# Optimization experiments

Measured on AMD Instinct MI355X. Metric: run time of the kernel, lower is better.

## Reference

```python
import jax, jax.numpy as jnp
import numpy as np

# Static conv config (matches init_kwargs)
STRIDE = (1, 1, 1)
PAD = (1, 1, 1)
DIL = (1, 1, 1)
DG = 1  # deformable groups


def setup_inputs() -> dict:
    key = jax.random.key(0)
    k1, k2, k3 = jax.random.split(key, 3)
    N, Cin, T, H, W = 2, 32, 8, 56, 56
    Cout, kT, kH, kW = 64, 3, 3, 3
    x = jax.random.normal(k1, (N, Cin, T, H, W), dtype=jnp.float32)
    # offset channels = DG * 3 * kT*kH*kW = 81 ; layout [N, dg*K*3, To, Ho, Wo]
    offset = jax.random.normal(k2, (N, DG * 3 * kT * kH * kW, T, H, W), dtype=jnp.float32)
    stdv = 1.0 / np.sqrt(Cin * kT * kH * kW)
    weight = jax.random.uniform(k3, (Cout, Cin, kT, kH, kW), dtype=jnp.float32, minval=-stdv, maxval=stdv)
    bias = jnp.zeros((Cout,), dtype=jnp.float32)
    return {"x": x, "offset": offset, "weight": weight, "bias": bias}


def _deform_conv3d(x, offset, weight, bias):
    N, C, T, H, W = x.shape
    Co, _, kT, kH, kW = weight.shape
    K = kT * kH * kW
    st, sh, sw = STRIDE
    pt_, ph_, pw_ = PAD
    dt_, dh_, dw_ = DIL
    To = (T + 2 * pt_ - (dt_ * (kT - 1) + 1)) // st + 1
    Ho = (H + 2 * ph_ - (dh_ * (kH - 1) + 1)) // sh + 1
    Wo = (W + 2 * pw_ - (dw_ * (kW - 1) + 1)) // sw + 1
    Cg = C // DG
    # offsets: [N, DG, K, 3(dt,dh,dw), To, Ho, Wo]
    off = offset.reshape(N, DG, K, 3, To, Ho, Wo)
    kt, kh, kw = [g.reshape(-1) for g in jnp.meshgrid(
        jnp.arange(kT), jnp.arange(kH), jnp.arange(kW), indexing='ij')]
    # base sampling grid per kernel tap: [K, To, Ho, Wo] via broadcasting
    bt = (jnp.arange(To) * st - pt_)[None, :, None, None] + (kt * dt_)[:, None, None, None]
    bh = (jnp.arange(Ho) * sh - ph_)[None, None, :, None] + (kh * dh_)[:, None, None, None]
    bw = (jnp.arange(Wo) * sw - pw_)[None, None, None, :] + (kw * dw_)[:, None, None, None]
    # fractional sampling positions: [N, DG, K, To, Ho, Wo]
    pt = bt[None, None] + off[:, :, :, 0]
    ph = bh[None, None] + off[:, :, :, 1]
    pw = bw[None, None] + off[:, :, :, 2]
    t0f, h0f, w0f = jnp.floor(pt), jnp.floor(ph), jnp.floor(pw)
    lt, lh, lw = pt - t0f, ph - h0f, pw - w0f
    t0 = t0f.astype(jnp.int32)
    h0 = h0f.astype(jnp.int32)
    w0 = w0f.astype(jnp.int32)
    x_flat = x.reshape(N, DG, Cg, T * H * W)
    acc = jnp.zeros((N, DG, Cg, K, To, Ho, Wo), dtype=x.dtype)
    for ct in (0, 1):
        ti = t0 + ct
        wt = lt if ct else (1.0 - lt)
        for ch in (0, 1):
            hi = h0 + ch
            wh = lh if ch else (1.0 - lh)
            for cw in (0, 1):
                wi = w0 + cw
                ww = lw if cw else (1.0 - lw)
                valid = ((ti >= 0) & (ti < T) & (hi >= 0) & (hi < H) & (wi >= 0) & (wi < W))
                idx = (jnp.clip(ti, 0, T - 1) * H + jnp.clip(hi, 0, H - 1)) * W + jnp.clip(wi, 0, W - 1)
                v = jnp.take_along_axis(x_flat, idx.reshape(N, DG, 1, -1), axis=3)
                v = v.reshape(N, DG, Cg, K, To, Ho, Wo)
                wgt = (wt * wh * ww * valid.astype(x.dtype))[:, :, None]  # [N,DG,1,K,To,Ho,Wo]
                acc = acc + v * wgt
    w_r = weight.reshape(Co, DG, Cg, K)
    out = jnp.einsum('ogck,ngcktuv->notuv', w_r, acc)
    if bias.size > 0:
        out = out + bias[None, :, None, None, None]
    return out


def reference(x, offset, weight, bias):
    return _deform_conv3d(x, offset, weight, bias)
```

## Files before the change

### kernel.cpp

```cpp
#include <hip/hip_runtime.h>
#include <hip/hip_fp16.h>

#define CIN   32
#define COUT  64
#define TT    8
#define HH    56
#define WW    56
#define KK    27
#define SP    (TT * HH * WW)
#define NB    2
#define NBLK  784
#define DBLK  1568
#define KSPLIT 14

typedef __attribute__((ext_vector_type(8))) _Float16 half8;
typedef __attribute__((ext_vector_type(4))) float    f32x4;

#define WF_OFF   0
#define XTH_OFF  (128 << 10)

__global__ __launch_bounds__(256) void prep_kernel(const float* __restrict__ x,
                                                   const float* __restrict__ w,
                                                   __half* __restrict__ xTh,
                                                   __half* __restrict__ wf) {
    const int b = blockIdx.x;
    const int t = threadIdx.x;
    if (b < NBLK) {
        __shared__ float sm[CIN][65];
        const int s0 = b * 64, n = s0 / SP, sp0 = s0 % SP;
#pragma unroll
        for (int it = 0; it < 8; ++it) {
            const int idx = it * 256 + t, c = idx >> 6, l = idx & 63;
            sm[c][l] = x[((size_t)n * CIN + c) * SP + sp0 + l];
        }
        __syncthreads();
#pragma unroll
        for (int it = 0; it < 4; ++it) {
            const int idx = it * 256 + t, l = idx >> 4, cp = idx & 15;
            ((__half2*)xTh)[((size_t)n * SP + sp0 + l) * (CIN / 2) + cp] =
                __floats2half2_rn(sm[2 * cp][l], sm[2 * cp + 1][l]);
        }
    } else {
        const int k = b - NBLK;
#pragma unroll
        for (int it = 0; it < 8; ++it) {
            const int idx  = it * 256 + t;
            const int j    = idx & 7;
            const int lane = (idx >> 3) & 63;
            const int ct   = (idx >> 9) & 3;
            const int co   = ct * 16 + (lane & 15);
            const int c    = (lane >> 4) * 8 + j;
            wf[(((size_t)k * 4 + ct) * 64 + lane) * 8 + j] =
                __float2half(w[((size_t)co * CIN + c) * KK + k]);
        }
    }
}

__global__ __launch_bounds__(256, 3) void dconv3d_kernel(const __half* __restrict__ xTh,
                                                         const float* __restrict__ off,
                                                         const __half* __restrict__ wf,
                                                         const float* __restrict__ bias,
                                                         float* __restrict__ out) {
    __shared__ __align__(16) char smem[81 * 32 * 4];
    float (*offs)[32] = reinterpret_cast<float(*)[32]>(smem);
    float (*cmb)[2][64] = reinterpret_cast<float(*)[2][64]>(smem);

    const int t    = threadIdx.x;
    const int lane = t & 63;
    const int wv   = t >> 6;
    const int wpos = wv & 1;
    const int half = wv >> 1;

    const int posI = lane >> 2;
    const int cgI  = lane & 3;
    const int jg   = lane >> 4;

    const int bp_addr = (((lane & 15) << 2) | jg) << 2;

    const int sb  = (blockIdx.x & 7) * 196 + (blockIdx.x >> 3);
    const int s0  = sb * 32;
    const int n   = s0 / SP;
    const int spb = s0 % SP;

    {
        const float* offbase = off + ((size_t)n * (3 * KK)) * SP + spb;
        for (int i = t; i < 81 * 8; i += 256) {
            const int row = i >> 3, q = i & 7;
            *(float4*)&offs[row][q * 4] = *(const float4*)(offbase + (size_t)row * SP + q * 4);
        }
    }
    __syncthreads();

    const int sp = spb + wpos * 16 + posI;
    const int to = sp / (HH * WW);
    const int hw = sp % (HH * WW);
    const int ho = hw / WW;
    const int wo = hw % WW;
    const int pl = wpos * 16 + posI;

    f32x4 acc[4];
#pragma unroll
    for (int ct = 0; ct < 4; ++ct)
#pragma unroll
        for (int r = 0; r < 4; ++r)
            acc[ct][r] = half ? 0.f : bias[ct * 16 + jg * 4 + r];

    const __half* xn = xTh + (size_t)n * SP * CIN;

    float4 g[2][8];
    float  cw[2][8];

    auto issue = [&](int k, int b) {
        const int kt  = k / 9;
        const int khh = (k / 3) % 3;
        const int kww = k % 3;

        const float pt_ = (float)(to - 1 + kt)  + offs[k * 3 + 0][pl];
        const float ph_ = (float)(ho - 1 + khh) + offs[k * 3 + 1][pl];
        const float pw_ = (float)(wo - 1 + kww) + offs[k * 3 + 2][pl];

        const float ft = floorf(pt_), fh = floorf(ph_), fw = floorf(pw_);
        const float lt = pt_ - ft, lh = ph_ - fh, lw = pw_ - fw;
        const int t0 = (int)ft, h0 = (int)fh, w0 = (int)fw;
        const int t1 = t0 + 1, h1 = h0 + 1, w1 = w0 + 1;

        float awt[2], awh[2], aww[2];
        int   it2[2], ih2[2], iw2[2];
        awt[0] = ((unsigned)t0 < TT) ? (1.f - lt) : 0.f;
        awt[1] = ((unsigned)t1 < TT) ? lt : 0.f;
        it2[0] = min(max(t0, 0), TT - 1);  it2[1] = min(max(t1, 0), TT - 1);
        awh[0] = ((unsigned)h0 < HH) ? (1.f - lh) : 0.f;
        awh[1] = ((unsigned)h1 < HH) ? lh : 0.f;
        ih2[0] = min(max(h0, 0), HH - 1);  ih2[1] = min(max(h1, 0), HH - 1);
        aww[0] = ((unsigned)w0 < WW) ? (1.f - lw) : 0.f;
        aww[1] = ((unsigned)w1 < WW) ? lw : 0.f;
        iw2[0] = min(max(w0, 0), WW - 1);  iw2[1] = min(max(w1, 0), WW - 1);

        const int dT   = (it2[1] - it2[0]) * (HH * WW);
        const int dH   = (ih2[1] - ih2[0]) * WW;
        const int dW   = iw2[1] - iw2[0];
        const int base = (it2[0] * HH + ih2[0]) * WW + iw2[0];

        int a[8];
        a[0] = base;           a[1] = base + dW;
        a[2] = base + dH;      a[3] = a[2] + dW;
        a[4] = base + dT;      a[5] = a[4] + dW;
        a[6] = a[4] + dH;      a[7] = a[6] + dW;
#pragma unroll
        for (int ci = 0; ci < 8; ++ci) {
            const int i0 = ci >> 2, i1 = (ci >> 1) & 1, i2 = ci & 1;
            cw[b][ci] = awt[i0] * awh[i1] * aww[i2];
        }
#pragma unroll
        for (int ci = 0; ci < 8; ++ci)
            g[b][ci] = *(const float4*)(xn + (size_t)a[ci] * CIN + cgI * 8);
    };

    auto consume = [&](int b, half8 af0, half8 af1, half8 af2, half8 af3) {
        __half2 vacc[4];
#pragma unroll
        for (int j = 0; j < 4; ++j) vacc[j] = __floats2half2_rn(0.f, 0.f);
#pragma unroll
        for (int ci = 0; ci < 8; ++ci) {
            const __half2* uh = (const __half2*)&g[b][ci];
            const __half2 cw2 = __float2half2_rn(cw[b][ci]);
            vacc[0] = __hfma2(cw2, uh[0], vacc[0]);
            vacc[1] = __hfma2(cw2, uh[1], vacc[1]);
            vacc[2] = __hfma2(cw2, uh[2], vacc[2]);
            vacc[3] = __hfma2(cw2, uh[3], vacc[3]);
        }
        union { __half2 h2[4]; int i[4]; half8 h8; } u, v;
#pragma unroll
        for (int d = 0; d < 4; ++d) u.h2[d] = vacc[d];
#pragma unroll
        for (int d = 0; d < 4; ++d)
            v.i[d] = __builtin_amdgcn_ds_bpermute(bp_addr, u.i[d]);
        const half8 bfrag = v.h8;
        acc[0] = __builtin_amdgcn_mfma_f32_16x16x32_f16(af0, bfrag, acc[0], 0, 0, 0);
        acc[1] = __builtin_amdgcn_mfma_f32_16x16x32_f16(af1, bfrag, acc[1], 0, 0, 0);
        acc[2] = __builtin_amdgcn_mfma_f32_16x16x32_f16(af2, bfrag, acc[2], 0, 0, 0);
        acc[3] = __builtin_amdgcn_mfma_f32_16x16x32_f16(af3, bfrag, acc[3], 0, 0, 0);
    };

    if (half == 0) {
        issue(0, 0);
#pragma unroll
        for (int k = 0; k < KSPLIT; ++k) {
            const int cur = k & 1;
            const __half* wp = wf + ((size_t)k * 256 + lane) * 8;
            const half8 af0 = *(const half8*)(wp);
            const half8 af1 = *(const half8*)(wp + 512);
            const half8 af2 = *(const half8*)(wp + 1024);
            const half8 af3 = *(const half8*)(wp + 1536);
            if (k + 1 < KSPLIT) issue(k + 1, cur ^ 1);
            consume(cur, af0, af1, af2, af3);
        }
    } else {
        issue(KSPLIT, 0);
#pragma unroll
        for (int k = KSPLIT; k < KK; ++k) {
            const int cur = (k - KSPLIT) & 1;
            const __half* wp = wf + ((size_t)k * 256 + lane) * 8;
            const half8 af0 = *(const half8*)(wp);
            const half8 af1 = *(const half8*)(wp + 512);
            const half8 af2 = *(const half8*)(wp + 1024);
            const half8 af3 = *(const half8*)(wp + 1536);
            if (k + 1 < KK) issue(k + 1, cur ^ 1);
            consume(cur, af0, af1, af2, af3);
        }
    }

    __syncthreads();
    if (half == 1) {
#pragma unroll
        for (int ct = 0; ct < 4; ++ct)
#pragma unroll
            for (int r = 0; r < 4; ++r) cmb[ct * 4 + r][wpos][lane] = acc[ct][r];
    }
    __syncthreads();
    if (half == 0) {
#pragma unroll
        for (int ct = 0; ct < 4; ++ct)
#pragma unroll
            for (int r = 0; r < 4; ++r) {
                const int co = ct * 16 + jg * 4 + r;
                out[((size_t)n * COUT + co) * SP + spb + wpos * 16 + (lane & 15)] =
                    acc[ct][r] + cmb[ct * 4 + r][wpos][lane];
            }
    }
}

extern "C" void kernel_launch(void* const* d_in, const int* in_sizes, int n_in,
                              void* d_out, int out_size, void* d_ws, size_t ws_size,
                              hipStream_t stream) {
    const float* x    = (const float*)d_in[0];
    const float* off  = (const float*)d_in[1];
    const float* w    = (const float*)d_in[2];
    const float* bias = (const float*)d_in[3];
    float* out        = (float*)d_out;

    __half* wf  = (__half*)((char*)d_ws + WF_OFF);
    __half* xTh = (__half*)((char*)d_ws + XTH_OFF);

    prep_kernel<<<NBLK + KK, 256, 0, stream>>>(x, w, xTh, wf);
    dconv3d_kernel<<<DBLK, 256, 0, stream>>>(xTh, off, wf, bias, out);
}
```

Measured before the change: 121.5 us.

## Remap lanes to MFMA B-fragment layout, drop bpermute, raise occupancy

Lanes are remapped so that each lane gathers the channel slice and position that it later feeds directly as its MFMA B fragment. This removes the four ds_bpermute cross-lane shuffles per kernel tap. The launch bounds minimum blocks per CU is raised from 3 to 4, and sched_barrier fences pin the prefetch issue between the weight loads and the consume step. The higher occupancy target may force register spills, and the fences limit how freely the compiler can interleave instructions.

Result: slower. 156.6 us (+28.9%).

```diff
diff --git a/kernel.cpp b/kernel.cpp
--- a/kernel.cpp
+++ b/kernel.cpp
@@ -56,7 +56,7 @@
     }
 }
 
-__global__ __launch_bounds__(256, 3) void dconv3d_kernel(const __half* __restrict__ xTh,
+__global__ __launch_bounds__(256, 4) void dconv3d_kernel(const __half* __restrict__ xTh,
                                                          const float* __restrict__ off,
                                                          const __half* __restrict__ wf,
                                                          const float* __restrict__ bias,
@@ -71,11 +71,8 @@
     const int wpos = wv & 1;
     const int half = wv >> 1;
 
-    const int posI = lane >> 2;
-    const int cgI  = lane & 3;
+    const int posI = lane & 15;
     const int jg   = lane >> 4;
-
-    const int bp_addr = (((lane & 15) << 2) | jg) << 2;
 
     const int sb  = (blockIdx.x & 7) * 196 + (blockIdx.x >> 3);
     const int s0  = sb * 32;
@@ -153,29 +150,23 @@
         }
 #pragma unroll
         for (int ci = 0; ci < 8; ++ci)
-            g[b][ci] = *(const float4*)(xn + (size_t)a[ci] * CIN + cgI * 8);
+            g[b][ci] = *(const float4*)(xn + (size_t)a[ci] * CIN + jg * 8);
     };
 
     auto consume = [&](int b, half8 af0, half8 af1, half8 af2, half8 af3) {
-        __half2 vacc[4];
-#pragma unroll
-        for (int j = 0; j < 4; ++j) vacc[j] = __floats2half2_rn(0.f, 0.f);
+        union { __half2 h2[4]; half8 h8; } u;
+        u.h2[0] = __floats2half2_rn(0.f, 0.f);
+        u.h2[1] = u.h2[0]; u.h2[2] = u.h2[0]; u.h2[3] = u.h2[0];
 #pragma unroll
         for (int ci = 0; ci < 8; ++ci) {
             const __half2* uh = (const __half2*)&g[b][ci];
             const __half2 cw2 = __float2half2_rn(cw[b][ci]);
-            vacc[0] = __hfma2(cw2, uh[0], vacc[0]);
-            vacc[1] = __hfma2(cw2, uh[1], vacc[1]);
-            vacc[2] = __hfma2(cw2, uh[2], vacc[2]);
-            vacc[3] = __hfma2(cw2, uh[3], vacc[3]);
-        }
-        union { __half2 h2[4]; int i[4]; half8 h8; } u, v;
-#pragma unroll
-        for (int d = 0; d < 4; ++d) u.h2[d] = vacc[d];
-#pragma unroll
-        for (int d = 0; d < 4; ++d)
-            v.i[d] = __builtin_amdgcn_ds_bpermute(bp_addr, u.i[d]);
-        const half8 bfrag = v.h8;
+            u.h2[0] = __hfma2(cw2, uh[0], u.h2[0]);
+            u.h2[1] = __hfma2(cw2, uh[1], u.h2[1]);
+            u.h2[2] = __hfma2(cw2, uh[2], u.h2[2]);
+            u.h2[3] = __hfma2(cw2, uh[3], u.h2[3]);
+        }
+        const half8 bfrag = u.h8;
         acc[0] = __builtin_amdgcn_mfma_f32_16x16x32_f16(af0, bfrag, acc[0], 0, 0, 0);
         acc[1] = __builtin_amdgcn_mfma_f32_16x16x32_f16(af1, bfrag, acc[1], 0, 0, 0);
         acc[2] = __builtin_amdgcn_mfma_f32_16x16x32_f16(af2, bfrag, acc[2], 0, 0, 0);
@@ -192,7 +183,9 @@
             const half8 af1 = *(const half8*)(wp + 512);
             const half8 af2 = *(const half8*)(wp + 1024);
             const half8 af3 = *(const half8*)(wp + 1536);
+            __builtin_amdgcn_sched_barrier(0);
             if (k + 1 < KSPLIT) issue(k + 1, cur ^ 1);
+            __builtin_amdgcn_sched_barrier(0);
             consume(cur, af0, af1, af2, af3);
         }
     } else {
@@ -205,7 +198,9 @@
             const half8 af1 = *(const half8*)(wp + 512);
             const half8 af2 = *(const half8*)(wp + 1024);
             const half8 af3 = *(const half8*)(wp + 1536);
+            __builtin_amdgcn_sched_barrier(0);
             if (k + 1 < KK) issue(k + 1, cur ^ 1);
+            __builtin_amdgcn_sched_barrier(0);
             consume(cur, af0, af1, af2, af3);
         }
     }
@@ -224,7 +219,7 @@
 #pragma unroll
             for (int r = 0; r < 4; ++r) {
                 const int co = ct * 16 + jg * 4 + r;
-                out[((size_t)n * COUT + co) * SP + spb + wpos * 16 + (lane & 15)] =
+                out[((size_t)n * COUT + co) * SP + spb + wpos * 16 + posI] =
                     acc[ct][r] + cmb[ct * 4 + r][wpos][lane];
             }
     }
```
